# Kernel optimization log

Measured on AMD Instinct MI355X. Metric: run time of the kernel, lower is better.

## Reference

```python
import jax, jax.numpy as jnp
import numpy as np

BZ, C, H, W = 4, 512, 64, 64

def setup_inputs() -> dict:
    key = jax.random.key(0)
    k1, k2 = jax.random.split(key)
    inp = jax.random.normal(k1, (BZ, C, H, W), dtype=jnp.float32)
    mask = jax.random.randint(k2, (BZ, 1, H, W), 0, 2, dtype=jnp.int32)  # 1 = hole
    return {"input": inp, "mask": mask}

def reference(input, mask):
    bz, c, h, w = input.shape
    c2 = c // 2
    hw = h * w
    former = input[:, :c2].reshape(bz, c2, hw)   # decoder features
    latter = input[:, c2:].reshape(bz, c2, hw)   # encoder skip features
    # flag: 1 where masked (hole). shift_sz=1, stride=1, mask_thred=1 => flag == mask
    flag = (mask.reshape(bz, hw) >= 1)
    # cosine similarity between all per-pixel latter features (normalize once)
    norm = jnp.sqrt(jnp.sum(latter * latter, axis=1, keepdims=True))
    lat_n = latter / (norm + 1e-8)
    sim = jnp.einsum('bci,bcj->bij', lat_n, lat_n)  # [bz, hw(query), hw(key)]
    # only known (non-masked) pixels are valid shift sources (keys)
    NEG = jnp.float32(-1e9)
    sim = jnp.where(flag[:, None, :], NEG, sim)
    src_idx = jnp.argmax(sim, axis=2)  # [bz, hw] best known source per pixel
    # shift: copy former feature from matched known pixel into masked positions
    shifted = jnp.take_along_axis(former, src_idx[:, None, :], axis=2)  # [bz, c2, hw]
    shifted = jnp.where(flag[:, None, :], shifted, jnp.float32(0.0))
    out = jnp.concatenate([former, latter, shifted], axis=1)  # [bz, 3*c2, hw]
    return out.reshape(bz, 3 * c2, h, w)
```

## Files before the change

### kernel.cpp

```cpp
#include <hip/hip_runtime.h>


#define HW 4096
#define C2 256
#define BZd 4
#define TQ 32
#define NK 2
#define BT 256
#define SLK 512
#define NSL_MAX 8
#define QT_MAX 128
#define P1_GRID 1024

__device__ __forceinline__ unsigned ordf(float f) {
  unsigned u = __float_as_uint(f);
  return (u & 0x80000000u) ? ~u : (u | 0x80000000u);
}

__device__ __forceinline__ unsigned long long shfl_down_u64(unsigned long long v, int off) {
  unsigned lo = (unsigned)v, hi = (unsigned)(v >> 32);
  lo = __shfl_down(lo, off, 64);
  hi = __shfl_down(hi, off, 64);
  return ((unsigned long long)hi << 32) | lo;
}

__global__ void prep_kernel(const float* __restrict__ in, const int* __restrict__ mask,
                            float* __restrict__ inv, int* __restrict__ qcnt,
                            int* __restrict__ kcnt, int* __restrict__ qlist,
                            int* __restrict__ klist, int* __restrict__ srcmap) {
  __shared__ int s[256];
  int bid = blockIdx.x, t = threadIdx.x;
  if (bid < 64) {
    int idx = bid * 256 + t;
    int b = idx >> 12, j = idx & (HW - 1);
    const float* p = in + ((size_t)b * 512 + C2) * HW + j;
    float ss = 0.f;
#pragma unroll 8
    for (int c = 0; c < C2; ++c) { float v = p[(size_t)c * HW]; ss = fmaf(v, v, ss); }
    inv[idx] = 1.0f / (sqrtf(ss) + 1e-8f);
  } else {
    int b = bid - 64;
    const int* m = mask + b * HW;
    int base = t * 16;
    int fl = 0, cq = 0;
#pragma unroll
    for (int i = 0; i < 16; ++i) { int f = (m[base + i] >= 1); fl |= f << i; cq += f; }
    s[t] = cq; __syncthreads();
    for (int off = 1; off < 256; off <<= 1) {
      int v = (t >= off) ? s[t - off] : 0;
      __syncthreads(); s[t] += v; __syncthreads();
    }
    int total = s[255];
    int qp = s[t] - cq;
    int kp = base - qp;
    for (int i = 0; i < 16; ++i) {
      int j = base + i;
      if ((fl >> i) & 1) qlist[b * HW + qp++] = j;
      else               klist[b * HW + kp++] = j;
      srcmap[b * HW + j] = -1;
    }
    if (t == 0) { qcnt[b] = total; kcnt[b] = HW - total; }
  }
}

__global__ void pack_kernel(const float* __restrict__ in, const float* __restrict__ inv,
                            const int* __restrict__ qcnt, const int* __restrict__ kcnt,
                            const int* __restrict__ qlist, const int* __restrict__ klist,
                            float* __restrict__ kpack, float* __restrict__ qpack) {
  int t = threadIdx.x;
  int x = blockIdx.x;
  int c = blockIdx.y, b = blockIdx.z;
  const float* lat = in + ((size_t)b * 512 + C2 + c) * HW;
  if (x < 4) {
    int kc = kcnt[b];
    const float* dn = inv + b * HW;
    int base = (x << 10) + (t << 2);
    float v[4];
#pragma unroll
    for (int r = 0; r < 4; ++r) {
      int kk = base + r;
      float val = 0.f;
      if (kk < kc) { int j = klist[b * HW + kk]; val = lat[j] * dn[j]; }
      v[r] = val;
    }
    float* dst = kpack + ((size_t)(b * C2 + c)) * HW + base;
    *(float4*)dst = make_float4(v[0], v[1], v[2], v[3]);
  } else {
    int qc = x - 4, nq = qcnt[b];
    float* dst = qpack + ((size_t)(b * C2 + c)) * HW;
#pragma unroll
    for (int r = 0; r < 4; ++r) {
      int jj = (qc << 10) + (r << 8) + t;
      float val = 0.f;
      if (jj < nq) val = lat[qlist[b * HW + jj]];
      dst[jj] = val;
    }
  }
}

__device__ __forceinline__ void decode_id(unsigned idx,
    int nt0, int nt1, int nt2,
    int q0, int q1, int q2, int q3,
    int k0c, int k1c, int k2c, int k3c,
    int& b, int& sl, int& qtile, int& kc) {
  int qtn;
  b = 0; qtn = q0; kc = k0c;
  if (idx >= (unsigned)nt0) {
    idx -= nt0; b = 1; qtn = q1; kc = k1c;
    if (idx >= (unsigned)nt1) {
      idx -= nt1; b = 2; qtn = q2; kc = k2c;
      if (idx >= (unsigned)nt2) { idx -= nt2; b = 3; qtn = q3; kc = k3c; }
    }
  }
  sl = (int)(idx / (unsigned)qtn);
  qtile = (int)(idx - (unsigned)sl * (unsigned)qtn);
}

template <int TQL>
__device__ __forceinline__ void run_item(
    const float* __restrict__ qpack, const float* __restrict__ kpack,
    unsigned long long* __restrict__ partials,
    unsigned long long (*red)[TQ],
    int b, int sl, int qtile, int qoff, int kc,
    int t, int lane, int wid) {
  int qstart = (qtile << 5) + qoff;
  int kbase = (sl << 9) + (t << 1);

  const float* qb = qpack + ((size_t)b * C2) * HW + qstart;
  const float* kcol = kpack + ((size_t)b * C2) * HW + kbase;

  float acc[NK][TQL];
#pragma unroll
  for (int r = 0; r < NK; ++r)
#pragma unroll
    for (int q = 0; q < TQL; ++q) acc[r][q] = 0.f;

  float2 k0 = *(const float2*)(kcol);
  float2 k1 = *(const float2*)(kcol + HW);
#pragma unroll 2
  for (int c = 0; c < C2; ++c) {
    float2 kq = k0;
    k0 = k1;
    int cp = c + 2; if (cp > C2 - 1) cp = C2 - 1;
    k1 = *(const float2*)(kcol + (size_t)cp * HW);
    float kv[NK] = {kq.x, kq.y};
    const float* qc_ = qb + (size_t)c * HW;
#pragma unroll
    for (int i = 0; i < TQL; ++i) {
      float qv = qc_[i];
#pragma unroll
      for (int r = 0; r < NK; ++r)
        acc[r][i] = fmaf(kv[r], qv, acc[r][i]);
    }
  }

#pragma unroll
  for (int q = 0; q < TQL; ++q) {
    unsigned long long v = 0ull;
#pragma unroll
    for (int r = 0; r < NK; ++r) {
      int kk = kbase + r;
      if (kk < kc) {
        unsigned long long pk =
            ((unsigned long long)ordf(acc[r][q]) << 32) | (unsigned)(0xFFFFFFFFu - (unsigned)kk);
        if (pk > v) v = pk;
      }
    }
#pragma unroll
    for (int off = 32; off >= 1; off >>= 1) {
      unsigned long long o = shfl_down_u64(v, off);
      if (o > v) v = o;
    }
    if (lane == 0) red[wid][q] = v;
  }
  __syncthreads();
  if (t < TQL) {
    unsigned long long v = red[0][t];
#pragma unroll
    for (int ww = 1; ww < 4; ++ww) if (red[ww][t] > v) v = red[ww][t];
    partials[(((size_t)b * NSL_MAX + sl) * QT_MAX + qtile) * TQ + qoff + t] = v;
  }
  __syncthreads();
}

__global__ __launch_bounds__(BT, 4) void argmax_pass1(
    const float* __restrict__ qpack, const float* __restrict__ kpack,
    const int* __restrict__ qcnt, const int* __restrict__ kcnt,
    unsigned long long* __restrict__ partials) {
  int k0c = kcnt[0], k1c = kcnt[1], k2c = kcnt[2], k3c = kcnt[3];
  int s0 = (k0c + SLK - 1) >> 9, s1 = (k1c + SLK - 1) >> 9;
  int s2 = (k2c + SLK - 1) >> 9, s3 = (k3c + SLK - 1) >> 9;
  int q0 = (qcnt[0] + TQ - 1) >> 5, q1 = (qcnt[1] + TQ - 1) >> 5;
  int q2 = (qcnt[2] + TQ - 1) >> 5, q3 = (qcnt[3] + TQ - 1) >> 5;
  int nt0 = q0 * s0, nt1 = q1 * s1, nt2 = q2 * s2, nt3 = q3 * s3;
  unsigned total = (unsigned)(nt0 + nt1 + nt2 + nt3);
  unsigned S = gridDim.x;
  unsigned F = total / S;
  unsigned fullN = F * S;
  unsigned R = total - fullN;

  int t = threadIdx.x;
  int lane = t & 63, wid = t >> 6;
  __shared__ unsigned long long red[4][TQ];

  for (unsigned w = blockIdx.x; w < fullN; w += S) {
    int b, sl, qtile, kc;
    decode_id(w, nt0, nt1, nt2, q0, q1, q2, q3, k0c, k1c, k2c, k3c, b, sl, qtile, kc);
    run_item<TQ>(qpack, kpack, partials, red, b, sl, qtile, 0, kc, t, lane, wid);
  }
  for (unsigned qi = blockIdx.x; qi < 4u * R; qi += S) {
    unsigned id = fullN + (qi >> 2);
    int sub = (int)(qi & 3u);
    int b, sl, qtile, kc;
    decode_id(id, nt0, nt1, nt2, q0, q1, q2, q3, k0c, k1c, k2c, k3c, b, sl, qtile, kc);
    run_item<8>(qpack, kpack, partials, red, b, sl, qtile, sub * 8, kc, t, lane, wid);
  }
}

__global__ void argmax_pass2(const unsigned long long* __restrict__ partials,
                             const int* __restrict__ qcnt, const int* __restrict__ kcnt,
                             const int* __restrict__ qlist, const int* __restrict__ klist,
                             int* __restrict__ srcmap) {
  int idx = blockIdx.x * 256 + threadIdx.x;
  int b = idx >> 12, qpos = idx & (HW - 1);
  if (qpos >= qcnt[b]) return;
  int kc = kcnt[b];
  int ns = (kc + SLK - 1) >> 9;
  int qtile = qpos >> 5, q = qpos & (TQ - 1);
  unsigned long long v = 0ull;
  for (int s = 0; s < ns; ++s) {
    unsigned long long p = partials[(((size_t)b * NSL_MAX + s) * QT_MAX + qtile) * TQ + q];
    if (p > v) v = p;
  }
  if (!v) return;
  int kk = (int)(0xFFFFFFFFu - (unsigned)(v & 0xFFFFFFFFull));
  srcmap[b * HW + qlist[b * HW + qpos]] = klist[b * HW + kk];
}

__global__ void out_kernel(const float* __restrict__ in, const int* __restrict__ srcmap,
                           float* __restrict__ out) {
  int bid = blockIdx.x;
  if (bid < 8192) {
    size_t idx = (size_t)bid * 256 + threadIdx.x;
    int b = (int)(idx >> 19);
    size_t r = idx & 524287;
    float4 v = ((const float4*)in)[((size_t)b << 19) + r];
    ((float4*)(out + (size_t)b * 768 * HW))[r] = v;
  } else {
    int idx = (bid - 8192) * 256 + threadIdx.x;
    int j = idx & (HW - 1);
    int c = (idx >> 12) & 255;
    int b = idx >> 20;
    int s = srcmap[b * HW + j];
    float v = (s >= 0) ? in[((size_t)b * 512 + c) * HW + s] : 0.f;
    out[((size_t)b * 768 + 512 + c) * HW + j] = v;
  }
}

extern "C" void kernel_launch(void* const* d_in, const int* in_sizes, int n_in,
                              void* d_out, int out_size, void* d_ws, size_t ws_size,
                              hipStream_t stream) {
  const float* in = (const float*)d_in[0];
  const int* mask = (const int*)d_in[1];
  float* out = (float*)d_out;

  unsigned long long* partials = (unsigned long long*)d_ws;
  float* kpack = (float*)(partials + (size_t)BZd * NSL_MAX * QT_MAX * TQ);
  float* qpack = kpack + (size_t)BZd * C2 * HW;
  float* inv = qpack + (size_t)BZd * C2 * HW;
  int* qlist = (int*)(inv + BZd * HW);
  int* klist = qlist + BZd * HW;
  int* srcmap = klist + BZd * HW;
  int* qcnt = srcmap + BZd * HW;
  int* kcnt = qcnt + BZd;

  hipLaunchKernelGGL(prep_kernel, dim3(64 + BZd), dim3(256), 0, stream,
                     in, mask, inv, qcnt, kcnt, qlist, klist, srcmap);
  hipLaunchKernelGGL(pack_kernel, dim3(8, C2, BZd), dim3(256), 0, stream,
                     in, inv, qcnt, kcnt, qlist, klist, kpack, qpack);
  hipLaunchKernelGGL(argmax_pass1, dim3(P1_GRID), dim3(BT), 0, stream,
                     qpack, kpack, qcnt, kcnt, partials);
  hipLaunchKernelGGL(argmax_pass2, dim3(BZd * HW / 256), dim3(256), 0, stream,
                     partials, qcnt, kcnt, qlist, klist, srcmap);
  hipLaunchKernelGGL(out_kernel, dim3(8192 + 16384), dim3(256), 0, stream,
                     in, srcmap, out);
}
```

Baseline: 267.4 us.

## Halve query tile and use atomic work-stealing scheduler in argmax pass

Shrinks the query tile from 32 to 16 and replaces the static grid-stride split, with its tail-splitting path, by a dynamic atomic ticket counter that blocks pull work items from until exhausted. The aim is better load balance across CUs and no tail imbalance. The cost is half as much key-load reuse per item, twice as many items and partials, plus an atomic and a barrier per item. The counter is reset in prep_kernel.

```diff
diff --git a/kernel.cpp b/kernel.cpp
--- a/kernel.cpp
+++ b/kernel.cpp
@@ -4,12 +4,12 @@
 #define HW 4096
 #define C2 256
 #define BZd 4
-#define TQ 32
+#define TQ 16
 #define NK 2
 #define BT 256
 #define SLK 512
 #define NSL_MAX 8
-#define QT_MAX 128
+#define QT16_MAX 256
 #define P1_GRID 1024
 
 __device__ __forceinline__ unsigned ordf(float f) {
@@ -27,7 +27,8 @@
 __global__ void prep_kernel(const float* __restrict__ in, const int* __restrict__ mask,
                             float* __restrict__ inv, int* __restrict__ qcnt,
                             int* __restrict__ kcnt, int* __restrict__ qlist,
-                            int* __restrict__ klist, int* __restrict__ srcmap) {
+                            int* __restrict__ klist, int* __restrict__ srcmap,
+                            unsigned* __restrict__ wcnt) {
   __shared__ int s[256];
   int bid = blockIdx.x, t = threadIdx.x;
   if (bid < 64) {
@@ -40,6 +41,7 @@
     inv[idx] = 1.0f / (sqrtf(ss) + 1e-8f);
   } else {
     int b = bid - 64;
+    if (b == 0 && t == 0) wcnt[0] = 0;
     const int* m = mask + b * HW;
     int base = t * 16;
     int fl = 0, cq = 0;
@@ -116,24 +118,23 @@
   qtile = (int)(idx - (unsigned)sl * (unsigned)qtn);
 }
 
-template <int TQL>
 __device__ __forceinline__ void run_item(
     const float* __restrict__ qpack, const float* __restrict__ kpack,
     unsigned long long* __restrict__ partials,
     unsigned long long (*red)[TQ],
-    int b, int sl, int qtile, int qoff, int kc,
+    int b, int sl, int qtile, int kc,
     int t, int lane, int wid) {
-  int qstart = (qtile << 5) + qoff;
+  int qstart = qtile << 4;
   int kbase = (sl << 9) + (t << 1);
 
   const float* qb = qpack + ((size_t)b * C2) * HW + qstart;
   const float* kcol = kpack + ((size_t)b * C2) * HW + kbase;
 
-  float acc[NK][TQL];
+  float acc[NK][TQ];
 #pragma unroll
   for (int r = 0; r < NK; ++r)
 #pragma unroll
-    for (int q = 0; q < TQL; ++q) acc[r][q] = 0.f;
+    for (int q = 0; q < TQ; ++q) acc[r][q] = 0.f;
 
   float2 k0 = *(const float2*)(kcol);
   float2 k1 = *(const float2*)(kcol + HW);
@@ -146,7 +147,7 @@
     float kv[NK] = {kq.x, kq.y};
     const float* qc_ = qb + (size_t)c * HW;
 #pragma unroll
-    for (int i = 0; i < TQL; ++i) {
+    for (int i = 0; i < TQ; ++i) {
       float qv = qc_[i];
 #pragma unroll
       for (int r = 0; r < NK; ++r)
@@ -155,7 +156,7 @@
   }
 
 #pragma unroll
-  for (int q = 0; q < TQL; ++q) {
+  for (int q = 0; q < TQ; ++q) {
     unsigned long long v = 0ull;
 #pragma unroll
     for (int r = 0; r < NK; ++r) {
@@ -174,11 +175,11 @@
     if (lane == 0) red[wid][q] = v;
   }
   __syncthreads();
-  if (t < TQL) {
+  if (t < TQ) {
     unsigned long long v = red[0][t];
 #pragma unroll
     for (int ww = 1; ww < 4; ++ww) if (red[ww][t] > v) v = red[ww][t];
-    partials[(((size_t)b * NSL_MAX + sl) * QT_MAX + qtile) * TQ + qoff + t] = v;
+    partials[(((size_t)b * NSL_MAX + sl) * QT16_MAX + qtile) * TQ + t] = v;
   }
   __syncthreads();
 }
@@ -186,34 +187,28 @@
 __global__ __launch_bounds__(BT, 4) void argmax_pass1(
     const float* __restrict__ qpack, const float* __restrict__ kpack,
     const int* __restrict__ qcnt, const int* __restrict__ kcnt,
-    unsigned long long* __restrict__ partials) {
+    unsigned long long* __restrict__ partials, unsigned* __restrict__ wcnt) {
   int k0c = kcnt[0], k1c = kcnt[1], k2c = kcnt[2], k3c = kcnt[3];
   int s0 = (k0c + SLK - 1) >> 9, s1 = (k1c + SLK - 1) >> 9;
   int s2 = (k2c + SLK - 1) >> 9, s3 = (k3c + SLK - 1) >> 9;
-  int q0 = (qcnt[0] + TQ - 1) >> 5, q1 = (qcnt[1] + TQ - 1) >> 5;
-  int q2 = (qcnt[2] + TQ - 1) >> 5, q3 = (qcnt[3] + TQ - 1) >> 5;
+  int q0 = (qcnt[0] + TQ - 1) >> 4, q1 = (qcnt[1] + TQ - 1) >> 4;
+  int q2 = (qcnt[2] + TQ - 1) >> 4, q3 = (qcnt[3] + TQ - 1) >> 4;
   int nt0 = q0 * s0, nt1 = q1 * s1, nt2 = q2 * s2, nt3 = q3 * s3;
   unsigned total = (unsigned)(nt0 + nt1 + nt2 + nt3);
-  unsigned S = gridDim.x;
-  unsigned F = total / S;
-  unsigned fullN = F * S;
-  unsigned R = total - fullN;
 
   int t = threadIdx.x;
   int lane = t & 63, wid = t >> 6;
   __shared__ unsigned long long red[4][TQ];
-
-  for (unsigned w = blockIdx.x; w < fullN; w += S) {
+  __shared__ unsigned sTicket;
+
+  for (;;) {
+    if (t == 0) sTicket = atomicAdd(wcnt, 1u);
+    __syncthreads();
+    unsigned w = sTicket;
+    if (w >= total) break;
     int b, sl, qtile, kc;
     decode_id(w, nt0, nt1, nt2, q0, q1, q2, q3, k0c, k1c, k2c, k3c, b, sl, qtile, kc);
-    run_item<TQ>(qpack, kpack, partials, red, b, sl, qtile, 0, kc, t, lane, wid);
-  }
-  for (unsigned qi = blockIdx.x; qi < 4u * R; qi += S) {
-    unsigned id = fullN + (qi >> 2);
-    int sub = (int)(qi & 3u);
-    int b, sl, qtile, kc;
-    decode_id(id, nt0, nt1, nt2, q0, q1, q2, q3, k0c, k1c, k2c, k3c, b, sl, qtile, kc);
-    run_item<8>(qpack, kpack, partials, red, b, sl, qtile, sub * 8, kc, t, lane, wid);
+    run_item(qpack, kpack, partials, red, b, sl, qtile, kc, t, lane, wid);
   }
 }
 
@@ -226,10 +221,10 @@
   if (qpos >= qcnt[b]) return;
   int kc = kcnt[b];
   int ns = (kc + SLK - 1) >> 9;
-  int qtile = qpos >> 5, q = qpos & (TQ - 1);
+  int qtile = qpos >> 4, q = qpos & (TQ - 1);
   unsigned long long v = 0ull;
   for (int s = 0; s < ns; ++s) {
-    unsigned long long p = partials[(((size_t)b * NSL_MAX + s) * QT_MAX + qtile) * TQ + q];
+    unsigned long long p = partials[(((size_t)b * NSL_MAX + s) * QT16_MAX + qtile) * TQ + q];
     if (p > v) v = p;
   }
   if (!v) return;
@@ -265,7 +260,7 @@
   float* out = (float*)d_out;
 
   unsigned long long* partials = (unsigned long long*)d_ws;
-  float* kpack = (float*)(partials + (size_t)BZd * NSL_MAX * QT_MAX * TQ);
+  float* kpack = (float*)(partials + (size_t)BZd * NSL_MAX * QT16_MAX * TQ);
   float* qpack = kpack + (size_t)BZd * C2 * HW;
   float* inv = qpack + (size_t)BZd * C2 * HW;
   int* qlist = (int*)(inv + BZd * HW);
@@ -273,13 +268,14 @@
   int* srcmap = klist + BZd * HW;
   int* qcnt = srcmap + BZd * HW;
   int* kcnt = qcnt + BZd;
+  unsigned* wcnt = (unsigned*)(kcnt + BZd);
 
   hipLaunchKernelGGL(prep_kernel, dim3(64 + BZd), dim3(256), 0, stream,
-                     in, mask, inv, qcnt, kcnt, qlist, klist, srcmap);
+                     in, mask, inv, qcnt, kcnt, qlist, klist, srcmap, wcnt);
   hipLaunchKernelGGL(pack_kernel, dim3(8, C2, BZd), dim3(256), 0, stream,
                      in, inv, qcnt, kcnt, qlist, klist, kpack, qpack);
   hipLaunchKernelGGL(argmax_pass1, dim3(P1_GRID), dim3(BT), 0, stream,
-                     qpack, kpack, qcnt, kcnt, partials);
+                     qpack, kpack, qcnt, kcnt, partials, wcnt);
   hipLaunchKernelGGL(argmax_pass2, dim3(BZd * HW / 256), dim3(256), 0, stream,
                      partials, qcnt, kcnt, qlist, klist, srcmap);
   hipLaunchKernelGGL(out_kernel, dim3(8192 + 16384), dim3(256), 0, stream,
```

Result: slower. 310.3 us (+16.0%).

## Stage rows in LDS for pack and output gathers, split norm reduction

Applied to the files above, without the earlier changes.

The norm computation in prep now splits the channel sum across four thread groups and reduces through shared memory, which quadruples the block count. The pack kernel stages each latter channel row and the inverse-norm row in LDS, then gathers key and query values from LDS with vectorized index loads and stores. The output kernel handles one channel row per block: it copies the row to the output and, for former channels, gathers the shifted values from an LDS copy instead of doing scattered global reads. The cost is 16–32 KB of LDS per block, which may limit occupancy.

```diff
diff --git a/kernel.cpp b/kernel.cpp
--- a/kernel.cpp
+++ b/kernel.cpp
@@ -28,18 +28,25 @@
                             float* __restrict__ inv, int* __restrict__ qcnt,
                             int* __restrict__ kcnt, int* __restrict__ qlist,
                             int* __restrict__ klist, int* __restrict__ srcmap) {
-  __shared__ int s[256];
   int bid = blockIdx.x, t = threadIdx.x;
-  if (bid < 64) {
-    int idx = bid * 256 + t;
+  if (bid < 256) {
+    __shared__ float sred[4][64];
+    int p = t & 63, g = t >> 6;
+    int idx = bid * 64 + p;
     int b = idx >> 12, j = idx & (HW - 1);
-    const float* p = in + ((size_t)b * 512 + C2) * HW + j;
+    const float* base = in + ((size_t)b * 512 + C2 + g * 64) * HW + j;
     float ss = 0.f;
 #pragma unroll 8
-    for (int c = 0; c < C2; ++c) { float v = p[(size_t)c * HW]; ss = fmaf(v, v, ss); }
-    inv[idx] = 1.0f / (sqrtf(ss) + 1e-8f);
+    for (int c = 0; c < 64; ++c) { float v = base[(size_t)c * HW]; ss = fmaf(v, v, ss); }
+    sred[g][p] = ss;
+    __syncthreads();
+    if (g == 0) {
+      float s0 = ((sred[0][p] + sred[1][p]) + sred[2][p]) + sred[3][p];
+      inv[idx] = 1.0f / (sqrtf(s0) + 1e-8f);
+    }
   } else {
-    int b = bid - 64;
+    int b = bid - 256;
+    __shared__ int s[256];
     const int* m = mask + b * HW;
     int base = t * 16;
     int fl = 0, cq = 0;
@@ -67,34 +74,40 @@
                             const int* __restrict__ qcnt, const int* __restrict__ kcnt,
                             const int* __restrict__ qlist, const int* __restrict__ klist,
                             float* __restrict__ kpack, float* __restrict__ qpack) {
+  __shared__ float slat[HW];
+  __shared__ float sinv[HW];
   int t = threadIdx.x;
-  int x = blockIdx.x;
-  int c = blockIdx.y, b = blockIdx.z;
-  const float* lat = in + ((size_t)b * 512 + C2 + c) * HW;
-  if (x < 4) {
-    int kc = kcnt[b];
-    const float* dn = inv + b * HW;
-    int base = (x << 10) + (t << 2);
-    float v[4];
-#pragma unroll
-    for (int r = 0; r < 4; ++r) {
-      int kk = base + r;
-      float val = 0.f;
-      if (kk < kc) { int j = klist[b * HW + kk]; val = lat[j] * dn[j]; }
-      v[r] = val;
-    }
-    float* dst = kpack + ((size_t)(b * C2 + c)) * HW + base;
-    *(float4*)dst = make_float4(v[0], v[1], v[2], v[3]);
-  } else {
-    int qc = x - 4, nq = qcnt[b];
-    float* dst = qpack + ((size_t)(b * C2 + c)) * HW;
-#pragma unroll
-    for (int r = 0; r < 4; ++r) {
-      int jj = (qc << 10) + (r << 8) + t;
-      float val = 0.f;
-      if (jj < nq) val = lat[qlist[b * HW + jj]];
-      dst[jj] = val;
-    }
+  int c = blockIdx.x, b = blockIdx.y;
+  const float4* lat4 = (const float4*)(in + ((size_t)b * 512 + C2 + c) * HW);
+  const float4* inv4 = (const float4*)(inv + (size_t)b * HW);
+#pragma unroll
+  for (int i = 0; i < 4; ++i) {
+    int p = i * 256 + t;
+    ((float4*)slat)[p] = lat4[p];
+    ((float4*)sinv)[p] = inv4[p];
+  }
+  int kc = kcnt[b], nq = qcnt[b];
+  const int* kl = klist + b * HW;
+  const int* ql = qlist + b * HW;
+  float* kdst = kpack + (size_t)(b * C2 + c) * HW;
+  float* qdst = qpack + (size_t)(b * C2 + c) * HW;
+  __syncthreads();
+#pragma unroll
+  for (int i = 0; i < 4; ++i) {
+    int jj = (i * 256 + t) * 4;
+    int4 k4 = *(const int4*)(kl + jj);
+    int4 q4 = *(const int4*)(ql + jj);
+    float4 kv, qv;
+    kv.x = (jj + 0 < kc) ? slat[k4.x] * sinv[k4.x] : 0.f;
+    kv.y = (jj + 1 < kc) ? slat[k4.y] * sinv[k4.y] : 0.f;
+    kv.z = (jj + 2 < kc) ? slat[k4.z] * sinv[k4.z] : 0.f;
+    kv.w = (jj + 3 < kc) ? slat[k4.w] * sinv[k4.w] : 0.f;
+    qv.x = (jj + 0 < nq) ? slat[q4.x] : 0.f;
+    qv.y = (jj + 1 < nq) ? slat[q4.y] : 0.f;
+    qv.z = (jj + 2 < nq) ? slat[q4.z] : 0.f;
+    qv.w = (jj + 3 < nq) ? slat[q4.w] : 0.f;
+    *(float4*)(kdst + jj) = kv;
+    *(float4*)(qdst + jj) = qv;
   }
 }
 
@@ -239,21 +252,35 @@
 
 __global__ void out_kernel(const float* __restrict__ in, const int* __restrict__ srcmap,
                            float* __restrict__ out) {
+  __shared__ float srow[HW];
   int bid = blockIdx.x;
-  if (bid < 8192) {
-    size_t idx = (size_t)bid * 256 + threadIdx.x;
-    int b = (int)(idx >> 19);
-    size_t r = idx & 524287;
-    float4 v = ((const float4*)in)[((size_t)b << 19) + r];
-    ((float4*)(out + (size_t)b * 768 * HW))[r] = v;
-  } else {
-    int idx = (bid - 8192) * 256 + threadIdx.x;
-    int j = idx & (HW - 1);
-    int c = (idx >> 12) & 255;
-    int b = idx >> 20;
-    int s = srcmap[b * HW + j];
-    float v = (s >= 0) ? in[((size_t)b * 512 + c) * HW + s] : 0.f;
-    out[((size_t)b * 768 + 512 + c) * HW + j] = v;
+  int b = bid >> 9, c = bid & 511;
+  int t = threadIdx.x;
+  const float4* src = (const float4*)(in + ((size_t)b * 512 + c) * HW);
+  float4* dst = (float4*)(out + ((size_t)b * 768 + c) * HW);
+#pragma unroll
+  for (int i = 0; i < 4; ++i) {
+    int p = i * 256 + t;
+    float4 v = src[p];
+    ((float4*)srow)[p] = v;
+    dst[p] = v;
+  }
+  if (c < 256) {
+    __syncthreads();
+    const int* sm = srcmap + b * HW;
+    float4* dst2 = (float4*)(out + ((size_t)b * 768 + 512 + c) * HW);
+#pragma unroll
+    for (int i = 0; i < 4; ++i) {
+      int p = i * 256 + t;
+      int j0 = p * 4;
+      int4 s4 = *(const int4*)(sm + j0);
+      float4 o;
+      o.x = (s4.x >= 0) ? srow[s4.x] : 0.f;
+      o.y = (s4.y >= 0) ? srow[s4.y] : 0.f;
+      o.z = (s4.z >= 0) ? srow[s4.z] : 0.f;
+      o.w = (s4.w >= 0) ? srow[s4.w] : 0.f;
+      dst2[p] = o;
+    }
   }
 }
 
@@ -274,14 +301,14 @@
   int* qcnt = srcmap + BZd * HW;
   int* kcnt = qcnt + BZd;
 
-  hipLaunchKernelGGL(prep_kernel, dim3(64 + BZd), dim3(256), 0, stream,
+  hipLaunchKernelGGL(prep_kernel, dim3(256 + BZd), dim3(256), 0, stream,
                      in, mask, inv, qcnt, kcnt, qlist, klist, srcmap);
-  hipLaunchKernelGGL(pack_kernel, dim3(8, C2, BZd), dim3(256), 0, stream,
+  hipLaunchKernelGGL(pack_kernel, dim3(C2, BZd), dim3(256), 0, stream,
                      in, inv, qcnt, kcnt, qlist, klist, kpack, qpack);
   hipLaunchKernelGGL(argmax_pass1, dim3(P1_GRID), dim3(BT), 0, stream,
                      qpack, kpack, qcnt, kcnt, partials);
   hipLaunchKernelGGL(argmax_pass2, dim3(BZd * HW / 256), dim3(256), 0, stream,
                      partials, qcnt, kcnt, qlist, klist, srcmap);
-  hipLaunchKernelGGL(out_kernel, dim3(8192 + 16384), dim3(256), 0, stream,
+  hipLaunchKernelGGL(out_kernel, dim3(BZd * 512), dim3(256), 0, stream,
                      in, srcmap, out);
 }
```

Measured after the change: 228.1 us. -14.7%, faster.
